# Kernel tuning notes

Measured on AMD Instinct MI355X. Metric: run time of the kernel, lower is better.

Reference implementation:

```python
import jax, jax.numpy as jnp
import numpy as np

BETA = 0.9
THRESH = 1.0
SLOPE = 50.0

@jax.custom_vjp
def spike(x):
    # heaviside with fast_sigmoid(slope=50) surrogate gradient
    return (x > 0).astype(x.dtype)

def _spike_fwd(x):
    return spike(x), x

def _spike_bwd(x, g):
    grad = g / (SLOPE * jnp.abs(x) + 1.0) ** 2
    return (grad,)

spike.defvjp(_spike_fwd, _spike_bwd)

def setup_inputs() -> dict:
    key = jax.random.key(0)
    ks = jax.random.split(key, 9)
    T, B, D, H, C = 100, 128, 2048, 2048, 100
    s_in, s_h = 1.0 / np.sqrt(D), 1.0 / np.sqrt(H)
    return {
        'x_seq': jax.random.normal(ks[0], (T, B, D), dtype=jnp.float32),
        'W1': jax.random.uniform(ks[1], (D, H), minval=-s_in, maxval=s_in, dtype=jnp.float32),
        'b1': jax.random.uniform(ks[2], (H,), minval=-s_in, maxval=s_in, dtype=jnp.float32),
        'W2': jax.random.uniform(ks[3], (H, H), minval=-s_h, maxval=s_h, dtype=jnp.float32),
        'b2': jax.random.uniform(ks[4], (H,), minval=-s_h, maxval=s_h, dtype=jnp.float32),
        'W3': jax.random.uniform(ks[5], (H, H), minval=-s_h, maxval=s_h, dtype=jnp.float32),
        'b3': jax.random.uniform(ks[6], (H,), minval=-s_h, maxval=s_h, dtype=jnp.float32),
        'Wo': jax.random.uniform(ks[7], (H, C), minval=-s_h, maxval=s_h, dtype=jnp.float32),
        'bo': jax.random.uniform(ks[8], (C,), minval=-s_h, maxval=s_h, dtype=jnp.float32),
    }

def _lif(cur, mem):
    # snntorch Leaky (reset-by-subtraction): reset uses previous membrane
    reset = (mem - THRESH > 0).astype(mem.dtype)
    mem_new = BETA * mem + cur - reset * THRESH
    spk = spike(mem_new - THRESH)
    return spk, mem_new

def reference(x_seq, W1, b1, W2, b2, W3, b3, Wo, bo):
    T, B, _ = x_seq.shape
    H = W1.shape[1]
    C = Wo.shape[1]
    mem0 = (jnp.zeros((B, H)), jnp.zeros((B, H)), jnp.zeros((B, H)), jnp.zeros((B, C)))
    spk_sum0 = jnp.zeros((B, C))

    def step(carry, x_t):
        (m1, m2, m3, mo), ssum = carry
        s1, m1 = _lif(x_t @ W1 + b1, m1)
        s2, m2 = _lif(s1 @ W2 + b2, m2)
        s3, m3 = _lif(s2 @ W3 + b3, m3)
        so, mo = _lif(s3 @ Wo + bo, mo)
        return ((m1, m2, m3, mo), ssum + so), None

    (_, spk_out_sum), _ = jax.lax.scan(step, (mem0, spk_sum0), x_seq)
    return spk_out_sum
```

## Files before the change

### kernel.cpp

```cpp
#include <hip/hip_runtime.h>

typedef short short8 __attribute__((ext_vector_type(8)));
typedef float f32x4 __attribute__((ext_vector_type(4)));
typedef int int4v __attribute__((ext_vector_type(4)));

#define TT 100
#define BB 128
#define HH 2048
#define CC 100
#define NBLK 256
#define CHUNK 10
#define NCH (TT / CHUNK)
#define NPHASE (NCH + 3)
#define SLOTW 8192

__device__ inline unsigned short f2bf(float f) {
  unsigned u = __float_as_uint(f);
  return (unsigned short)((u + 0x7FFF + ((u >> 16) & 1)) >> 16);
}
__device__ inline float bf2f(unsigned short b) {
  return __uint_as_float((unsigned)b << 16);
}

__global__ __launch_bounds__(256) void transpose_cvt(
    const float* __restrict__ W, unsigned short* __restrict__ Wt)
{
  __shared__ float t[32][33];
  int n0 = blockIdx.x * 32, k0 = blockIdx.y * 32;
  int tx = threadIdx.x, ty = threadIdx.y;
  #pragma unroll
  for (int j = 0; j < 4; ++j)
    t[ty + 8 * j][tx] = W[(size_t)(k0 + ty + 8 * j) * HH + n0 + tx];
  __syncthreads();
  #pragma unroll
  for (int j = 0; j < 4; ++j)
    Wt[(size_t)(n0 + ty + 8 * j) * HH + k0 + tx] = f2bf(t[tx][ty + 8 * j]);
}

__global__ __launch_bounds__(512) void cvt_x(
    const float* __restrict__ x, unsigned short* __restrict__ xb, long n8)
{
  long i = (long)blockIdx.x * blockDim.x + threadIdx.x;
  if (i >= n8) return;
  const float4* p = (const float4*)x + i * 2;
  float4 a = p[0], b = p[1];
  short8 pv;
  pv[0] = (short)f2bf(a.x); pv[1] = (short)f2bf(a.y);
  pv[2] = (short)f2bf(a.z); pv[3] = (short)f2bf(a.w);
  pv[4] = (short)f2bf(b.x); pv[5] = (short)f2bf(b.y);
  pv[6] = (short)f2bf(b.z); pv[7] = (short)f2bf(b.w);
  *(short8*)(xb + i * 8) = pv;
}

__global__ __launch_bounds__(256) void gemm_big_bf16(
    const unsigned short* __restrict__ Ab, const unsigned short* __restrict__ Wt,
    const float* __restrict__ bias, unsigned short* __restrict__ cur)
{
  __shared__ unsigned short As[128 * 128];
  __shared__ unsigned short Bs[64 * 128];
  const int tid = threadIdx.x;
  const int w = tid >> 6, l = tid & 63;
  const int wm = w & 1, wn = w >> 1;
  const int c16 = l & 15, g = l >> 4;
  const int n0 = blockIdx.x * 64, m0 = blockIdx.y * 128;
  f32x4 acc[4][2] = {};

  for (int k0 = 0; k0 < 2048; k0 += 128) {
    #pragma unroll
    for (int i = 0; i < 8; ++i) {
      int gg = tid + i * 256;
      int r = gg >> 4, gi = gg & 15;
      int kb = (gi * 16) ^ ((r & 7) << 4);
      const char* src = (const char*)(Ab + (size_t)(m0 + r) * HH + k0) + kb;
      *(int4v*)((char*)As + r * 256 + kb) = *(const int4v*)src;
    }
    #pragma unroll
    for (int i = 0; i < 4; ++i) {
      int gg = tid + i * 256;
      int r = gg >> 4, gi = gg & 15;
      int kb = (gi * 16) ^ ((r & 7) << 4);
      const char* bsrc = (const char*)(Wt + (size_t)(n0 + r) * HH + k0) + kb;
      *(int4v*)((char*)Bs + r * 256 + kb) = *(const int4v*)bsrc;
    }
    __syncthreads();
    #pragma unroll
    for (int kk = 0; kk < 4; ++kk) {
      int koff = (kk * 4 + g) * 16;
      short8 a[4], b[2];
      #pragma unroll
      for (int mi = 0; mi < 4; ++mi) {
        int mr = wm * 64 + mi * 16 + c16;
        a[mi] = *(short8*)((char*)As + mr * 256 + (koff ^ ((mr & 7) << 4)));
      }
      #pragma unroll
      for (int ni = 0; ni < 2; ++ni) {
        int nr = wn * 32 + ni * 16 + c16;
        b[ni] = *(short8*)((char*)Bs + nr * 256 + (koff ^ ((nr & 7) << 4)));
      }
      #pragma unroll
      for (int mi = 0; mi < 4; ++mi)
        #pragma unroll
        for (int ni = 0; ni < 2; ++ni)
          acc[mi][ni] = __builtin_amdgcn_mfma_f32_16x16x32_bf16(
              a[mi], b[ni], acc[mi][ni], 0, 0, 0);
    }
    __syncthreads();
  }
  #pragma unroll
  for (int mi = 0; mi < 4; ++mi)
    #pragma unroll
    for (int ni = 0; ni < 2; ++ni) {
      int col = n0 + wn * 32 + ni * 16 + c16;
      int rbase = m0 + wm * 64 + mi * 16 + g * 4;
      float bv = bias[col];
      #pragma unroll
      for (int j = 0; j < 4; ++j)
        cur[(size_t)(rbase + j) * HH + col] = f2bf(acc[mi][ni][j] + bv);
    }
}

__global__ __launch_bounds__(256) void gemm_big_f32(
    const float* __restrict__ A, const unsigned short* __restrict__ Wt,
    const float* __restrict__ bias, unsigned short* __restrict__ cur)
{
  __shared__ unsigned short As[128 * 128];
  __shared__ unsigned short Bs[64 * 128];
  const int tid = threadIdx.x;
  const int w = tid >> 6, l = tid & 63;
  const int wm = w & 1, wn = w >> 1;
  const int c16 = l & 15, g = l >> 4;
  const int n0 = blockIdx.x * 64, m0 = blockIdx.y * 128;
  f32x4 acc[4][2] = {};

  for (int k0 = 0; k0 < 2048; k0 += 128) {
    #pragma unroll
    for (int i = 0; i < 8; ++i) {
      int gg = tid + i * 256;
      int r = gg >> 4, gi = gg & 15;
      int kb = (gi * 16) ^ ((r & 7) << 4);
      const float* src = A + (size_t)(m0 + r) * HH + k0 + (kb >> 1);
      float4 f0 = *(const float4*)src, f1 = *(const float4*)(src + 4);
      short8 pv;
      pv[0] = (short)f2bf(f0.x); pv[1] = (short)f2bf(f0.y);
      pv[2] = (short)f2bf(f0.z); pv[3] = (short)f2bf(f0.w);
      pv[4] = (short)f2bf(f1.x); pv[5] = (short)f2bf(f1.y);
      pv[6] = (short)f2bf(f1.z); pv[7] = (short)f2bf(f1.w);
      *(int4v*)((char*)As + r * 256 + kb) = *(int4v*)&pv;
    }
    #pragma unroll
    for (int i = 0; i < 4; ++i) {
      int gg = tid + i * 256;
      int r = gg >> 4, gi = gg & 15;
      int kb = (gi * 16) ^ ((r & 7) << 4);
      const char* bsrc = (const char*)(Wt + (size_t)(n0 + r) * HH + k0) + kb;
      *(int4v*)((char*)Bs + r * 256 + kb) = *(const int4v*)bsrc;
    }
    __syncthreads();
    #pragma unroll
    for (int kk = 0; kk < 4; ++kk) {
      int koff = (kk * 4 + g) * 16;
      short8 a[4], b[2];
      #pragma unroll
      for (int mi = 0; mi < 4; ++mi) {
        int mr = wm * 64 + mi * 16 + c16;
        a[mi] = *(short8*)((char*)As + mr * 256 + (koff ^ ((mr & 7) << 4)));
      }
      #pragma unroll
      for (int ni = 0; ni < 2; ++ni) {
        int nr = wn * 32 + ni * 16 + c16;
        b[ni] = *(short8*)((char*)Bs + nr * 256 + (koff ^ ((nr & 7) << 4)));
      }
      #pragma unroll
      for (int mi = 0; mi < 4; ++mi)
        #pragma unroll
        for (int ni = 0; ni < 2; ++ni)
          acc[mi][ni] = __builtin_amdgcn_mfma_f32_16x16x32_bf16(
              a[mi], b[ni], acc[mi][ni], 0, 0, 0);
    }
    __syncthreads();
  }
  #pragma unroll
  for (int mi = 0; mi < 4; ++mi)
    #pragma unroll
    for (int ni = 0; ni < 2; ++ni) {
      int col = n0 + wn * 32 + ni * 16 + c16;
      int rbase = m0 + wm * 64 + mi * 16 + g * 4;
      float bv = bias[col];
      #pragma unroll
      for (int j = 0; j < 4; ++j)
        cur[(size_t)(rbase + j) * HH + col] = f2bf(acc[mi][ni][j] + bv);
    }
}

__global__ void init_kernel(unsigned* flags, int n)
{
  int i = blockIdx.x * blockDim.x + threadIdx.x;
  int stride = gridDim.x * blockDim.x;
  for (int j = i; j < n; j += stride) flags[j] = 0u;
}

#define MM(WORD, HF, SIDX) { \
    unsigned h_ = (HF) ? ((unsigned)(WORD) >> 16) : ((unsigned)(WORD) & 0xFFFFu); \
    int4v af_; \
    af_[0] = (int)(((h_ & 15u) * 0x204081u) & 0x01010101u); \
    af_[1] = (int)((((h_ >> 4) & 15u) * 0x204081u) & 0x01010101u); \
    af_[2] = (int)((((h_ >> 8) & 15u) * 0x204081u) & 0x01010101u); \
    af_[3] = (int)(((h_ >> 12) * 0x204081u) & 0x01010101u); \
    int4v bq_ = *(const int4v*)(bpan + bbase + (((SIDX) * 64) ^ bswz)); \
    acc_ = __builtin_amdgcn_mfma_i32_16x16x64_i8(af_, bq_, acc_, 0, 0, 0); }

#define STEP8(ACV, CH) \
    MM(ACV[CH][0], 0, CH * 8 + 0) MM(ACV[CH][0], 1, CH * 8 + 1) \
    MM(ACV[CH][1], 0, CH * 8 + 2) MM(ACV[CH][1], 1, CH * 8 + 3) \
    MM(ACV[CH][2], 0, CH * 8 + 4) MM(ACV[CH][2], 1, CH * 8 + 5) \
    MM(ACV[CH][3], 0, CH * 8 + 6) MM(ACV[CH][3], 1, CH * 8 + 7)

#define LOADN(AN, TN) { \
    const char* sb_ = (const char*)(sinb + (size_t)(TN) * SLOTW); \
    AN[0] = *(const int4v*)(sb_ + abyte + 0 * 64); \
    AN[1] = *(const int4v*)(sb_ + abyte + 1 * 64); \
    AN[2] = *(const int4v*)(sb_ + abyte + 2 * 64); \
    AN[3] = *(const int4v*)(sb_ + abyte + 3 * 64); }

#define STEPB(AC, AN, T, DOPRE) { \
    if (DOPRE) LOADN(AN, (T) + 1); \
    int4v acc_ = {0, 0, 0, 0}; \
    STEP8(AC, 0) STEP8(AC, 1) STEP8(AC, 2) STEP8(AC, 3) \
    unsigned long long bal0_, bal1_, bal2_, bal3_; \
    { float cv_ = (float)acc_[0] * scl + bv, mo_ = memb[0]; \
      float mn_ = 0.9f * mo_ + cv_ - ((mo_ > 1.f) ? 1.f : 0.f); \
      memb[0] = mn_; bal0_ = __ballot((int)(mn_ > 1.f)); } \
    { float cv_ = (float)acc_[1] * scl + bv, mo_ = memb[1]; \
      float mn_ = 0.9f * mo_ + cv_ - ((mo_ > 1.f) ? 1.f : 0.f); \
      memb[1] = mn_; bal1_ = __ballot((int)(mn_ > 1.f)); } \
    { float cv_ = (float)acc_[2] * scl + bv, mo_ = memb[2]; \
      float mn_ = 0.9f * mo_ + cv_ - ((mo_ > 1.f) ? 1.f : 0.f); \
      memb[2] = mn_; bal2_ = __ballot((int)(mn_ > 1.f)); } \
    { float cv_ = (float)acc_[3] * scl + bv, mo_ = memb[3]; \
      float mn_ = 0.9f * mo_ + cv_ - ((mo_ > 1.f) ? 1.f : 0.f); \
      memb[3] = mn_; bal3_ = __ballot((int)(mn_ > 1.f)); } \
    if (c16 == 0) { \
      unsigned short* so_ = (unsigned short*)(soutb + (size_t)(T) * SLOTW); \
      int rb_ = w * 16 + g * 4; \
      so_[(rb_ + 0) * 128 + ppos] = (unsigned short)((bal0_ >> (g * 16)) & 0xFFFFull); \
      so_[(rb_ + 1) * 128 + ppos] = (unsigned short)((bal1_ >> (g * 16)) & 0xFFFFull); \
      so_[(rb_ + 2) * 128 + ppos] = (unsigned short)((bal2_ >> (g * 16)) & 0xFFFFull); \
      so_[(rb_ + 3) * 128 + ppos] = (unsigned short)((bal3_ >> (g * 16)) & 0xFFFFull); \
    } }

__global__ __launch_bounds__(512, 1) void snn_persist(
    const unsigned short* __restrict__ cur1,
    const float* __restrict__ W2, const float* __restrict__ b2,
    const float* __restrict__ W3, const float* __restrict__ b3,
    const float* __restrict__ Wo, const float* __restrict__ bo,
    unsigned* __restrict__ s1b, unsigned* __restrict__ s2b,
    unsigned* __restrict__ s3b,
    float* __restrict__ outsum, unsigned* __restrict__ flags,
    unsigned* __restrict__ go)
{
  __shared__ char bpan[16 * 2048];
  __shared__ unsigned sow[CHUNK * 64];
  __shared__ unsigned long long swm[CHUNK];

  const int blk = blockIdx.x, tid = threadIdx.x;
  const int w = tid >> 6, l = tid & 63;
  const int c16 = l & 15, g = l >> 4;
  const bool isL2 = blk < 128;
  const int panel = blk & 127;
  const int n0c = panel * 16;
  const float* Wsrc = isL2 ? W2 : W3;
  const float* bias = isL2 ? b2 : b3;
  const int col = n0c + c16;

  float mx = 0.f;
  for (int s = 0; s < 32; ++s) {
    int kb = s * 64 + g * 16;
    #pragma unroll
    for (int e = 0; e < 16; ++e)
      mx = fmaxf(mx, fabsf(Wsrc[(size_t)(kb + e) * HH + col]));
  }
  mx = fmaxf(mx, __shfl_xor(mx, 16));
  mx = fmaxf(mx, __shfl_xor(mx, 32));
  const float scl = mx * (1.f / 127.f);
  const float rsc = (mx > 0.f) ? (127.f / mx) : 0.f;
  const float bv = bias[col];

  {
    int c = tid & 15, kg = tid >> 4;
    #pragma unroll
    for (int j = 0; j < 4; ++j) {
      int k16 = kg * 64 + j * 16;
      int4v q = {0, 0, 0, 0};
      #pragma unroll
      for (int e = 0; e < 16; ++e) {
        float v = Wsrc[(size_t)(k16 + e) * HH + col];
        int qi = (int)rintf(v * rsc);
        qi = qi > 127 ? 127 : (qi < -127 ? -127 : qi);
        q[e >> 2] |= (qi & 0xFF) << ((e & 3) * 8);
      }
      *(int4v*)(bpan + c * 2048 + (k16 ^ ((c & 7) << 4))) = q;
    }
  }
  __syncthreads();

  const int bbase = c16 * 2048 + g * 16;
  const int bswz = (c16 & 7) << 4;

  const int ppos = ((panel >> 5) << 5) + ((panel & 3) << 3) + ((panel >> 2) & 7);
  const int arow = w * 16 + c16;
  const int abyte = arow * 256 + g * 16;

  f32x4 m1reg = {0.f, 0.f, 0.f, 0.f};
  f32x4 memb = {0.f, 0.f, 0.f, 0.f};
  float memo = 0.f, osumo = 0.f;
  const float boc = (!isL2 && tid < CC) ? bo[tid] : 0.f;

  for (int p = 0; p < NPHASE; ++p) {
    if (isL2 && p < NCH) {
      unsigned cw0[CHUNK], cw1[CHUNK];
      #pragma unroll
      for (int st = 0; st < CHUNK; ++st) {
        const unsigned* cp = (const unsigned*)(cur1 +
            ((size_t)(p * CHUNK + st) * BB + blk) * HH) + tid * 2;
        cw0[st] = cp[0]; cw1[st] = cp[1];
      }
      #pragma unroll
      for (int st = 0; st < CHUNK; ++st) {
        float cv[4] = { bf2f((unsigned short)(cw0[st] & 0xFFFF)),
                        bf2f((unsigned short)(cw0[st] >> 16)),
                        bf2f((unsigned short)(cw1[st] & 0xFFFF)),
                        bf2f((unsigned short)(cw1[st] >> 16)) };
        unsigned nib = 0;
        #pragma unroll
        for (int j = 0; j < 4; ++j) {
          float mo = m1reg[j];
          float mn = 0.9f * mo + cv[j] - ((mo > 1.f) ? 1.f : 0.f);
          m1reg[j] = mn;
          nib |= (mn > 1.f ? 1u : 0u) << j;
        }
        unsigned v = nib;
        v |= ((unsigned)__shfl_xor((int)v, 1)) << 4;
        v |= ((unsigned)__shfl_xor((int)v, 2)) << 8;
        v |= ((unsigned)__shfl_xor((int)v, 4)) << 16;
        if ((tid & 7) == 0) {
          int w8 = tid >> 3;
          int q0 = ((w8 >> 4) << 5) + ((w8 & 1) << 4) + ((w8 & 15) >> 1);
          unsigned short* so = (unsigned short*)(s1b +
              (size_t)(p * CHUNK + st) * SLOTW) + blk * 128;
          so[q0] = (unsigned short)(v & 0xFFFF);
          so[q0 + 8] = (unsigned short)(v >> 16);
        }
      }
    }

    int tch = p - (isL2 ? 1 : 2);
    if (tch >= 0 && tch < NCH) {
      const unsigned* sinb = isL2 ? s1b : s2b;
      unsigned* soutb = isL2 ? s2b : s3b;
      int4v A0[4], A1[4];
      LOADN(A0, tch * CHUNK);
      for (int st2 = 0; st2 < CHUNK; st2 += 2) {
        const int t0 = tch * CHUNK + st2;
        STEPB(A0, A1, t0, 1)
        STEPB(A1, A0, t0 + 1, st2 + 1 < CHUNK - 1)
      }
    }

    int oc = p - 3;
    if (!isL2 && oc >= 0 && oc < NCH) {
      int r = blk - 128;
      for (int i = tid; i < CHUNK * 64; i += 512)
        sow[i] = s3b[(size_t)(oc * CHUNK + (i >> 6)) * SLOTW + r * 64 + (i & 63)];
      __syncthreads();
      if (tid < CHUNK) {
        unsigned long long m = 0;
        for (int wd = 0; wd < 64; ++wd)
          if (sow[tid * 64 + wd]) m |= 1ull << wd;
        swm[tid] = m;
      }
      __syncthreads();
      if (tid < CC) {
        #pragma unroll 1
        for (int st = 0; st < CHUNK; ++st) {
          float curv = boc;
          unsigned long long m = swm[st];
          while (m) {
            int wd = (int)__ffsll((long long)m) - 1; m &= m - 1;
            unsigned wv2 = sow[st * 64 + wd];
            #pragma unroll
            for (int hf = 0; hf < 2; ++hf) {
              unsigned hv = hf ? (wv2 >> 16) : (wv2 & 0xFFFFu);
              int P = wd * 2 + hf;
              int kap = ((P >> 5) << 5) + ((P & 7) << 2) + ((P >> 3) & 3);
              while (hv) {
                int b = (int)__ffs(hv) - 1; hv &= hv - 1;
                curv += Wo[(size_t)(kap * 16 + b) * CC + tid];
              }
            }
          }
          float mo = memo;
          float mn = 0.9f * mo + curv - ((mo > 1.f) ? 1.f : 0.f);
          memo = mn;
          if (mn > 1.f) osumo += 1.f;
        }
      }
      __syncthreads();
    }

    if (p < NPHASE - 1) {
      unsigned gen = (unsigned)(p + 1);
      __syncthreads();
      if (tid == 0)
        __hip_atomic_store(&flags[blk * 32], gen, __ATOMIC_RELEASE,
                           __HIP_MEMORY_SCOPE_AGENT);
      if (blk == 0) {
        if (tid < NBLK) {
          int guard = 0;
          while (__hip_atomic_load(&flags[tid * 32], __ATOMIC_ACQUIRE,
                                   __HIP_MEMORY_SCOPE_AGENT) < gen) {
            __builtin_amdgcn_s_sleep(2);
            if (++guard > (1 << 22)) break;
          }
        }
        __syncthreads();
        if (tid == 0)
          __hip_atomic_store(go, gen, __ATOMIC_RELEASE,
                             __HIP_MEMORY_SCOPE_AGENT);
      } else {
        if (tid == 0) {
          int guard = 0;
          while (__hip_atomic_load(go, __ATOMIC_ACQUIRE,
                                   __HIP_MEMORY_SCOPE_AGENT) < gen) {
            __builtin_amdgcn_s_sleep(4);
            if (++guard > (1 << 22)) break;
          }
        }
        __syncthreads();
      }
    }
  }

  if (!isL2 && tid < CC)
    outsum[(blk - 128) * CC + tid] = osumo;
}

extern "C" void kernel_launch(void* const* d_in, const int* in_sizes, int n_in,
                              void* d_out, int out_size, void* d_ws, size_t ws_size,
                              hipStream_t stream)
{
  const float* x  = (const float*)d_in[0];
  const float* W1 = (const float*)d_in[1];
  const float* b1 = (const float*)d_in[2];
  const float* W2 = (const float*)d_in[3];
  const float* b2 = (const float*)d_in[4];
  const float* W3 = (const float*)d_in[5];
  const float* b3 = (const float*)d_in[6];
  const float* Wo = (const float*)d_in[7];
  const float* bo = (const float*)d_in[8];
  float* out = (float*)d_out;

  unsigned* flags = (unsigned*)d_ws;
  unsigned* go = flags + 8192;
  unsigned* s1b = flags + 16384;
  unsigned* s2b = s1b + (size_t)TT * SLOTW;
  unsigned* s3b = s2b + (size_t)TT * SLOTW;
  unsigned short* Wt1 = (unsigned short*)(s3b + (size_t)TT * SLOTW);
  unsigned short* cur1 = Wt1 + (size_t)HH * HH;
  unsigned short* xb = cur1 + (size_t)TT * BB * HH;
  size_t need_xb = (size_t)((char*)(xb + (size_t)TT * BB * HH) - (char*)d_ws);

  hipLaunchKernelGGL(init_kernel, dim3(32), dim3(256), 0, stream, flags, 16384);
  hipLaunchKernelGGL(transpose_cvt, dim3(64, 64), dim3(32, 8), 0, stream, W1, Wt1);
  if (ws_size >= need_xb) {
    long n8 = (long)TT * BB * HH / 8;
    hipLaunchKernelGGL(cvt_x, dim3((unsigned)((n8 + 511) / 512)), dim3(512),
                       0, stream, x, xb, n8);
    hipLaunchKernelGGL(gemm_big_bf16, dim3(HH / 64, (TT * BB) / 128), dim3(256),
                       0, stream, xb, Wt1, b1, cur1);
  } else {
    hipLaunchKernelGGL(gemm_big_f32, dim3(HH / 64, (TT * BB) / 128), dim3(256),
                       0, stream, x, Wt1, b1, cur1);
  }
  hipLaunchKernelGGL(snn_persist, dim3(NBLK), dim3(512), 0, stream,
                     cur1, W2, b2, W3, b3, Wo, bo,
                     s1b, s2b, s3b, out, flags, go);
}
```

Baseline: 798.5 us.

## Spread layer-1 LIF across all blocks, double chunk size, split MFMA accumulators

The layer-1 LIF/spike-packing work, previously done only by the L2 blocks, is now split across every block: each block takes half a batch row with two neurons per thread. CHUNK goes from 10 to 20, so there are fewer pipeline phases and fewer cross-block handoffs. The int8 MFMA chain now uses two independent accumulators that are summed at the end, which shortens the dependency chain. The risks are higher register pressure from the larger chunk and a longer pipeline fill and drain per phase.

```diff
diff --git a/kernel.cpp b/kernel.cpp
--- a/kernel.cpp
+++ b/kernel.cpp
@@ -9,7 +9,7 @@
 #define HH 2048
 #define CC 100
 #define NBLK 256
-#define CHUNK 10
+#define CHUNK 20
 #define NCH (TT / CHUNK)
 #define NPHASE (NCH + 3)
 #define SLOTW 8192
@@ -199,7 +199,7 @@
   for (int j = i; j < n; j += stride) flags[j] = 0u;
 }
 
-#define MM(WORD, HF, SIDX) { \
+#define MM(WORD, HF, SIDX, ACCV) { \
     unsigned h_ = (HF) ? ((unsigned)(WORD) >> 16) : ((unsigned)(WORD) & 0xFFFFu); \
     int4v af_; \
     af_[0] = (int)(((h_ & 15u) * 0x204081u) & 0x01010101u); \
@@ -207,13 +207,13 @@
     af_[2] = (int)((((h_ >> 8) & 15u) * 0x204081u) & 0x01010101u); \
     af_[3] = (int)(((h_ >> 12) * 0x204081u) & 0x01010101u); \
     int4v bq_ = *(const int4v*)(bpan + bbase + (((SIDX) * 64) ^ bswz)); \
-    acc_ = __builtin_amdgcn_mfma_i32_16x16x64_i8(af_, bq_, acc_, 0, 0, 0); }
-
-#define STEP8(ACV, CH) \
-    MM(ACV[CH][0], 0, CH * 8 + 0) MM(ACV[CH][0], 1, CH * 8 + 1) \
-    MM(ACV[CH][1], 0, CH * 8 + 2) MM(ACV[CH][1], 1, CH * 8 + 3) \
-    MM(ACV[CH][2], 0, CH * 8 + 4) MM(ACV[CH][2], 1, CH * 8 + 5) \
-    MM(ACV[CH][3], 0, CH * 8 + 6) MM(ACV[CH][3], 1, CH * 8 + 7)
+    ACCV = __builtin_amdgcn_mfma_i32_16x16x64_i8(af_, bq_, ACCV, 0, 0, 0); }
+
+#define STEP8(ACV, CH, ACCV) \
+    MM(ACV[CH][0], 0, CH * 8 + 0, ACCV) MM(ACV[CH][0], 1, CH * 8 + 1, ACCV) \
+    MM(ACV[CH][1], 0, CH * 8 + 2, ACCV) MM(ACV[CH][1], 1, CH * 8 + 3, ACCV) \
+    MM(ACV[CH][2], 0, CH * 8 + 4, ACCV) MM(ACV[CH][2], 1, CH * 8 + 5, ACCV) \
+    MM(ACV[CH][3], 0, CH * 8 + 6, ACCV) MM(ACV[CH][3], 1, CH * 8 + 7, ACCV)
 
 #define LOADN(AN, TN) { \
     const char* sb_ = (const char*)(sinb + (size_t)(TN) * SLOTW); \
@@ -224,19 +224,21 @@
 
 #define STEPB(AC, AN, T, DOPRE) { \
     if (DOPRE) LOADN(AN, (T) + 1); \
-    int4v acc_ = {0, 0, 0, 0}; \
-    STEP8(AC, 0) STEP8(AC, 1) STEP8(AC, 2) STEP8(AC, 3) \
+    int4v acc0_ = {0, 0, 0, 0}, acc1_ = {0, 0, 0, 0}; \
+    STEP8(AC, 0, acc0_) STEP8(AC, 1, acc0_) \
+    STEP8(AC, 2, acc1_) STEP8(AC, 3, acc1_) \
+    int4v accs_ = acc0_ + acc1_; \
     unsigned long long bal0_, bal1_, bal2_, bal3_; \
-    { float cv_ = (float)acc_[0] * scl + bv, mo_ = memb[0]; \
+    { float cv_ = (float)accs_[0] * scl + bv, mo_ = memb[0]; \
       float mn_ = 0.9f * mo_ + cv_ - ((mo_ > 1.f) ? 1.f : 0.f); \
       memb[0] = mn_; bal0_ = __ballot((int)(mn_ > 1.f)); } \
-    { float cv_ = (float)acc_[1] * scl + bv, mo_ = memb[1]; \
+    { float cv_ = (float)accs_[1] * scl + bv, mo_ = memb[1]; \
       float mn_ = 0.9f * mo_ + cv_ - ((mo_ > 1.f) ? 1.f : 0.f); \
       memb[1] = mn_; bal1_ = __ballot((int)(mn_ > 1.f)); } \
-    { float cv_ = (float)acc_[2] * scl + bv, mo_ = memb[2]; \
+    { float cv_ = (float)accs_[2] * scl + bv, mo_ = memb[2]; \
       float mn_ = 0.9f * mo_ + cv_ - ((mo_ > 1.f) ? 1.f : 0.f); \
       memb[2] = mn_; bal2_ = __ballot((int)(mn_ > 1.f)); } \
-    { float cv_ = (float)acc_[3] * scl + bv, mo_ = memb[3]; \
+    { float cv_ = (float)accs_[3] * scl + bv, mo_ = memb[3]; \
       float mn_ = 0.9f * mo_ + cv_ - ((mo_ > 1.f) ? 1.f : 0.f); \
       memb[3] = mn_; bal3_ = __ballot((int)(mn_ > 1.f)); } \
     if (c16 == 0) { \
@@ -310,45 +312,44 @@
   const int arow = w * 16 + c16;
   const int abyte = arow * 256 + g * 16;
 
-  f32x4 m1reg = {0.f, 0.f, 0.f, 0.f};
+  const int l1row = panel;
+  const int l1colbase = (blk >> 7) * 1024;
+  const int l1kap = (blk >> 7) * 64 + (tid >> 3);
+  const int l1pos = (l1kap & ~31) + ((l1kap & 3) << 3) + ((l1kap >> 2) & 7);
+
+  float m1a = 0.f, m1b = 0.f;
   f32x4 memb = {0.f, 0.f, 0.f, 0.f};
   float memo = 0.f, osumo = 0.f;
   const float boc = (!isL2 && tid < CC) ? bo[tid] : 0.f;
 
   for (int p = 0; p < NPHASE; ++p) {
-    if (isL2 && p < NCH) {
-      unsigned cw0[CHUNK], cw1[CHUNK];
-      #pragma unroll
-      for (int st = 0; st < CHUNK; ++st) {
-        const unsigned* cp = (const unsigned*)(cur1 +
-            ((size_t)(p * CHUNK + st) * BB + blk) * HH) + tid * 2;
-        cw0[st] = cp[0]; cw1[st] = cp[1];
-      }
-      #pragma unroll
-      for (int st = 0; st < CHUNK; ++st) {
-        float cv[4] = { bf2f((unsigned short)(cw0[st] & 0xFFFF)),
-                        bf2f((unsigned short)(cw0[st] >> 16)),
-                        bf2f((unsigned short)(cw1[st] & 0xFFFF)),
-                        bf2f((unsigned short)(cw1[st] >> 16)) };
-        unsigned nib = 0;
+    if (p < NCH) {
+      #pragma unroll
+      for (int half = 0; half < 2; ++half) {
+        unsigned cw[10];
         #pragma unroll
-        for (int j = 0; j < 4; ++j) {
-          float mo = m1reg[j];
-          float mn = 0.9f * mo + cv[j] - ((mo > 1.f) ? 1.f : 0.f);
-          m1reg[j] = mn;
-          nib |= (mn > 1.f ? 1u : 0u) << j;
+        for (int st = 0; st < 10; ++st) {
+          int t = p * CHUNK + half * 10 + st;
+          cw[st] = *((const unsigned*)(cur1 +
+                     ((size_t)t * BB + l1row) * HH + l1colbase) + tid);
         }
-        unsigned v = nib;
-        v |= ((unsigned)__shfl_xor((int)v, 1)) << 4;
-        v |= ((unsigned)__shfl_xor((int)v, 2)) << 8;
-        v |= ((unsigned)__shfl_xor((int)v, 4)) << 16;
-        if ((tid & 7) == 0) {
-          int w8 = tid >> 3;
-          int q0 = ((w8 >> 4) << 5) + ((w8 & 1) << 4) + ((w8 & 15) >> 1);
-          unsigned short* so = (unsigned short*)(s1b +
-              (size_t)(p * CHUNK + st) * SLOTW) + blk * 128;
-          so[q0] = (unsigned short)(v & 0xFFFF);
-          so[q0 + 8] = (unsigned short)(v >> 16);
+        #pragma unroll
+        for (int st = 0; st < 10; ++st) {
+          int t = p * CHUNK + half * 10 + st;
+          float c0 = bf2f((unsigned short)(cw[st] & 0xFFFF));
+          float c1 = bf2f((unsigned short)(cw[st] >> 16));
+          float mn0 = 0.9f * m1a + c0 - ((m1a > 1.f) ? 1.f : 0.f);
+          float mn1 = 0.9f * m1b + c1 - ((m1b > 1.f) ? 1.f : 0.f);
+          m1a = mn0; m1b = mn1;
+          unsigned v = (mn0 > 1.f ? 1u : 0u) | (mn1 > 1.f ? 2u : 0u);
+          v |= ((unsigned)__shfl_xor((int)v, 1)) << 2;
+          v |= ((unsigned)__shfl_xor((int)v, 2)) << 4;
+          v |= ((unsigned)__shfl_xor((int)v, 4)) << 8;
+          if ((tid & 7) == 0) {
+            unsigned short* so = (unsigned short*)(s1b + (size_t)t * SLOTW)
+                                 + l1row * 128;
+            so[l1pos] = (unsigned short)v;
+          }
         }
       }
     }
```

After: 712.7 us. 1.12x faster.
